# Kernel tuning notes

Measured on AMD Instinct MI355X. Metric: run time of the kernel, lower is better.

## Reference

```python
import jax, jax.numpy as jnp
import numpy as np
from functools import partial

GAMMA = 1.0
LAM = 1.0
N_ITER = 60  # fixed iteration count for the projected-gradient dual fused-lasso solver
GROUP_TOL = 1e-6


def _gfl_solve_row(x, A, lam):
    """Graph fused lasso: argmin_y 0.5||y-x||^2 + lam*sum_ij A_ij |y_i - y_j|.
    Solved by projected gradient ascent on the dual (edge flows z_ij in [-lam*A_ij, lam*A_ij]).
    x: [N], A: [N, N] -> y: [N]
    """
    N = x.shape[0]
    w = lam * A
    step = jnp.asarray(1.0 / (2.0 * N), dtype=x.dtype)

    def body(z, _):
        y = x - jnp.sum(z, axis=1) + jnp.sum(z, axis=0)  # primal from flows
        z = jnp.clip(z + step * (y[:, None] - y[None, :]), -w, w)
        return z, None

    z, _ = jax.lax.scan(body, jnp.zeros_like(A), None, length=N_ITER)
    return x - jnp.sum(z, axis=1) + jnp.sum(z, axis=0)


@partial(jax.custom_vjp, nondiff_argnums=(2,))
def gfusedlasso(x, A, lam):
    # x: [B, N], A: [B, N, N]
    return jax.vmap(_gfl_solve_row, in_axes=(0, 0, None))(x, A, lam)


def _gfl_fwd(x, A, lam):
    out = gfusedlasso(x, A, lam)
    return out, out


def _gfl_bwd(lam, out, g):
    # Faithful to backward_gfusedmax_torch_1D: average grad over groups of equal outputs.
    eq = (jnp.abs(out[:, :, None] - out[:, None, :]) < GROUP_TOL).astype(g.dtype)  # [B,N,N]
    grad_x = jnp.einsum('bij,bj->bi', eq, g) / jnp.sum(eq, axis=2)
    return grad_x, jnp.zeros_like(eq)  # no gradient defined for A (matches torch)


gfusedlasso.defvjp(_gfl_fwd, _gfl_bwd)


def sparsemax(x, axis=-1):
    # torch_sparsemax.forward with gamma=1.0
    N = x.shape[axis]
    x_sorted = jnp.flip(jnp.sort(x, axis=axis), axis=axis)  # descending
    cumsum = jnp.cumsum(x_sorted, axis=axis)
    k = jnp.arange(1, N + 1, dtype=x.dtype)  # broadcast along last axis
    mask = (1.0 + k * x_sorted > cumsum).astype(x.dtype)
    tau = (jnp.sum(x_sorted * mask, axis=axis, keepdims=True) - 1.0) / jnp.sum(mask, axis=axis, keepdims=True)
    return jnp.maximum(x - tau, 0.0)


def setup_inputs() -> dict:
    key = jax.random.key(0)
    kx, ka = jax.random.split(key)
    B, N = 4096, 128
    x = jax.random.normal(kx, (B, N), dtype=jnp.float32)
    A = jax.random.uniform(ka, (B, N, N), dtype=jnp.float32)
    return {"x": x, "A": A}


def reference(x, A):
    # Gfusedmax.forward: x/gamma -> gfusedlasso(lam/gamma) -> sparsemax(gamma=1)
    xg = x / GAMMA
    fused = gfusedlasso(xg, A, LAM / GAMMA)
    return sparsemax(fused, axis=-1)
```

## Files before the change

kernel.cpp:

```cpp
#include <hip/hip_runtime.h>

#define N 128
#define NITER 60
#define PSTR 132

typedef float v2f __attribute__((ext_vector_type(2)));
typedef float v4f __attribute__((ext_vector_type(4)));

__global__ __launch_bounds__(256, 1)
void gfusedmax_kernel(const float* __restrict__ x,
                      const float* __restrict__ A,
                      float* __restrict__ out)
{
    const int b   = blockIdx.x;
    const int tid = threadIdx.x;
    const int tr  = tid >> 4;
    const int tc  = tid & 15;
    const int i0  = tr * 8;
    const int j0  = tc * 8;

    __shared__ float rowpart[16 * PSTR];
    __shared__ float colpart[16 * PSTR];
    __shared__ float yv[N];
    __shared__ float sorted[N];
    __shared__ float red[8];

    const float step = 1.0f / 256.0f;

    v2f w2[8][4];
    v2f z2[8][4];
    const float* Ab = A + (size_t)b * N * N;
    #pragma unroll
    for (int r = 0; r < 8; ++r) {
        const v4f* src = (const v4f*)(Ab + (size_t)(i0 + r) * N + j0);
        v4f p0 = src[0];
        v4f p1 = src[1];
        w2[r][0] = p0.lo; w2[r][1] = p0.hi;
        w2[r][2] = p1.lo; w2[r][3] = p1.hi;
        #pragma unroll
        for (int cp = 0; cp < 4; ++cp) z2[r][cp] = (v2f)0.0f;
    }

    float xi = 0.0f;
    if (tid < N) xi = x[(size_t)b * N + tid];

    v2f pr2[8], pc2[4];
    #pragma unroll
    for (int r = 0; r < 8; ++r) pr2[r] = (v2f)0.0f;
    #pragma unroll
    for (int cp = 0; cp < 4; ++cp) pc2[cp] = (v2f)0.0f;

    float yfin = 0.0f;

    for (int it = 0; it <= NITER; ++it) {
        #pragma unroll
        for (int r = 0; r < 8; ++r)
            rowpart[tc * PSTR + i0 + r] = pr2[r].x + pr2[r].y;
        v2f* cp_dst = (v2f*)&colpart[tr * PSTR + j0];
        #pragma unroll
        for (int cp = 0; cp < 4; ++cp) cp_dst[cp] = pc2[cp];
        __syncthreads();

        if (tid < N) {
            float rs = 0.0f, cs = 0.0f;
            #pragma unroll
            for (int k = 0; k < 16; ++k) rs += rowpart[k * PSTR + tid];
            #pragma unroll
            for (int k = 0; k < 16; ++k) cs += colpart[k * PSTR + tid];
            float y = xi - rs + cs;
            yfin = y;
            yv[tid] = (it == NITER) ? y : step * y;
        }
        __syncthreads();
        if (it == NITER) break;

        v2f drs[8], ec2[4];
        #pragma unroll
        for (int r = 0; r < 8; ++r) drs[r] = (v2f)yv[i0 + r];
        const v2f* yv2 = (const v2f*)yv;
        #pragma unroll
        for (int cp = 0; cp < 4; ++cp) ec2[cp] = yv2[tc * 4 + cp];
        #pragma unroll
        for (int r = 0; r < 8; ++r) pr2[r] = (v2f)0.0f;
        #pragma unroll
        for (int cp = 0; cp < 4; ++cp) pc2[cp] = (v2f)0.0f;
        #pragma unroll
        for (int r = 0; r < 8; ++r) {
            #pragma unroll
            for (int cp = 0; cp < 4; ++cp) {
                v2f t  = (z2[r][cp] + drs[r]) - ec2[cp];
                v2f wv = w2[r][cp];
                v2f zn;
                zn.x = __builtin_amdgcn_fmed3f(t.x, -wv.x, wv.x);
                zn.y = __builtin_amdgcn_fmed3f(t.y, -wv.y, wv.y);
                z2[r][cp] = zn;
                pr2[r]  += zn;
                pc2[cp] += zn;
            }
        }
    }

    float v = yfin;
    if (tid < N) {
        int rk = 0;
        for (int k = 0; k < N; ++k) {
            float u = yv[k];
            rk += (u > v) || (u == v && k < tid);
        }
        sorted[rk] = v;
    }
    __syncthreads();

    float s = 0.0f, csum = 0.0f;
    if (tid < N) {
        s = sorted[tid];
        for (int m = 0; m < N; ++m) {
            float t = sorted[m];
            if (m <= tid) csum += t;
        }
    }
    bool mask = (tid < N) && (1.0f + (float)(tid + 1) * s > csum);
    float aRed = mask ? s : 0.0f;
    float bRed = mask ? 1.0f : 0.0f;
    #pragma unroll
    for (int off = 32; off >= 1; off >>= 1) {
        aRed += __shfl_down(aRed, off, 64);
        bRed += __shfl_down(bRed, off, 64);
    }
    const int wid = tid >> 6;
    if ((tid & 63) == 0) { red[wid * 2] = aRed; red[wid * 2 + 1] = bRed; }
    __syncthreads();
    const float tau = (red[0] + red[2] + red[4] + red[6] - 1.0f)
                    / (red[1] + red[3] + red[5] + red[7]);
    if (tid < N) out[(size_t)b * N + tid] = fmaxf(v - tau, 0.0f);
}

extern "C" void kernel_launch(void* const* d_in, const int* in_sizes, int n_in,
                              void* d_out, int out_size, void* d_ws, size_t ws_size,
                              hipStream_t stream) {
    const float* x = (const float*)d_in[0];
    const float* A = (const float*)d_in[1];
    float* out = (float*)d_out;
    const int B = in_sizes[0] / N;
    gfusedmax_kernel<<<B, 256, 0, stream>>>(x, A, out);
}
```

Before: 877.5 us.

## Interleave two batch rows per block to overlap reductions with clip updates

Each block now handles two batch rows and alternates between them. While one row's z update runs, the same threads gather the other row's row and column partial sums from shared memory, which halves the barriers per row-iteration and hides reduction latency. The sort and sparsemax epilogue uses all 256 threads, one half per row. The cost is doubled register state per thread (z and w for two rows) and half as many blocks, so occupancy and spilling become a risk.

```diff
diff --git a/kernel.cpp b/kernel.cpp
--- a/kernel.cpp
+++ b/kernel.cpp
@@ -2,124 +2,160 @@
 
 #define N 128
 #define NITER 60
-#define PSTR 132
+#define RPS 129
+#define CPS 130
 
 typedef float v2f __attribute__((ext_vector_type(2)));
 typedef float v4f __attribute__((ext_vector_type(4)));
 
-__global__ __launch_bounds__(256, 1)
+template<int Q, int P>
+__device__ __forceinline__ void window_step(
+    v2f (&z2)[2][8][4], const v2f (&w2)[2][8][4],
+    float (&RP)[2][16 * RPS], float (&CP)[2][16 * CPS],
+    float (&YV)[2][N],
+    int tid, int tr, int tc, int i0, int j0,
+    float xiP, bool storeCond, bool rawStore)
+{
+    const float step = 1.0f / 256.0f;
+
+    v2f drs[8], ec2[4], pr2[8], pc2[4];
+    #pragma unroll
+    for (int r = 0; r < 8; ++r) drs[r] = (v2f)YV[Q][i0 + r];
+    const v2f* yv2 = (const v2f*)YV[Q];
+    #pragma unroll
+    for (int cp = 0; cp < 4; ++cp) ec2[cp] = yv2[tc * 4 + cp];
+
+    float rtmp[16], ctmp[16];
+    const int ridx = tid & (N - 1);
+    if (tid < N) {
+        #pragma unroll
+        for (int k = 0; k < 16; ++k) rtmp[k] = RP[P][k * RPS + ridx];
+        #pragma unroll
+        for (int k = 0; k < 16; ++k) ctmp[k] = CP[P][k * CPS + ridx];
+    }
+
+    #pragma unroll
+    for (int r = 0; r < 8; ++r) pr2[r] = (v2f)0.0f;
+    #pragma unroll
+    for (int cp = 0; cp < 4; ++cp) pc2[cp] = (v2f)0.0f;
+
+    #pragma unroll
+    for (int r = 0; r < 8; ++r) {
+        #pragma unroll
+        for (int cp = 0; cp < 4; ++cp) {
+            v2f t  = (z2[Q][r][cp] + drs[r]) - ec2[cp];
+            v2f wv = w2[Q][r][cp];
+            v2f zn;
+            zn.x = __builtin_amdgcn_fmed3f(t.x, -wv.x, wv.x);
+            zn.y = __builtin_amdgcn_fmed3f(t.y, -wv.y, wv.y);
+            z2[Q][r][cp] = zn;
+            pr2[r]  += zn;
+            pc2[cp] += zn;
+        }
+    }
+
+    #pragma unroll
+    for (int r = 0; r < 8; ++r)
+        RP[Q][tc * RPS + i0 + r] = pr2[r].x + pr2[r].y;
+    v2f* cd = (v2f*)&CP[Q][tr * CPS + j0];
+    #pragma unroll
+    for (int cp = 0; cp < 4; ++cp) cd[cp] = pc2[cp];
+
+    if (storeCond) {
+        float rs = 0.0f, cs = 0.0f;
+        #pragma unroll
+        for (int k = 0; k < 16; ++k) rs += rtmp[k];
+        #pragma unroll
+        for (int k = 0; k < 16; ++k) cs += ctmp[k];
+        float y = xiP - rs + cs;
+        YV[P][tid] = rawStore ? y : step * y;
+    }
+}
+
+__global__ __launch_bounds__(256, 2)
 void gfusedmax_kernel(const float* __restrict__ x,
                       const float* __restrict__ A,
                       float* __restrict__ out)
 {
-    const int b   = blockIdx.x;
+    const int b0  = blockIdx.x * 2;
     const int tid = threadIdx.x;
     const int tr  = tid >> 4;
     const int tc  = tid & 15;
     const int i0  = tr * 8;
     const int j0  = tc * 8;
 
-    __shared__ float rowpart[16 * PSTR];
-    __shared__ float colpart[16 * PSTR];
-    __shared__ float yv[N];
-    __shared__ float sorted[N];
-    __shared__ float red[8];
+    __shared__ float RP[2][16 * RPS];
+    __shared__ __align__(16) float CP[2][16 * CPS];
+    __shared__ __align__(16) float YV[2][N];
+    __shared__ float sorted[2][N];
+    __shared__ float red[2][4];
 
     const float step = 1.0f / 256.0f;
 
-    v2f w2[8][4];
-    v2f z2[8][4];
-    const float* Ab = A + (size_t)b * N * N;
+    v2f w2[2][8][4];
+    v2f z2[2][8][4];
     #pragma unroll
-    for (int r = 0; r < 8; ++r) {
-        const v4f* src = (const v4f*)(Ab + (size_t)(i0 + r) * N + j0);
-        v4f p0 = src[0];
-        v4f p1 = src[1];
-        w2[r][0] = p0.lo; w2[r][1] = p0.hi;
-        w2[r][2] = p1.lo; w2[r][3] = p1.hi;
-        #pragma unroll
-        for (int cp = 0; cp < 4; ++cp) z2[r][cp] = (v2f)0.0f;
-    }
-
-    float xi = 0.0f;
-    if (tid < N) xi = x[(size_t)b * N + tid];
-
-    v2f pr2[8], pc2[4];
-    #pragma unroll
-    for (int r = 0; r < 8; ++r) pr2[r] = (v2f)0.0f;
-    #pragma unroll
-    for (int cp = 0; cp < 4; ++cp) pc2[cp] = (v2f)0.0f;
-
-    float yfin = 0.0f;
-
-    for (int it = 0; it <= NITER; ++it) {
-        #pragma unroll
-        for (int r = 0; r < 8; ++r)
-            rowpart[tc * PSTR + i0 + r] = pr2[r].x + pr2[r].y;
-        v2f* cp_dst = (v2f*)&colpart[tr * PSTR + j0];
-        #pragma unroll
-        for (int cp = 0; cp < 4; ++cp) cp_dst[cp] = pc2[cp];
-        __syncthreads();
-
-        if (tid < N) {
-            float rs = 0.0f, cs = 0.0f;
-            #pragma unroll
-            for (int k = 0; k < 16; ++k) rs += rowpart[k * PSTR + tid];
-            #pragma unroll
-            for (int k = 0; k < 16; ++k) cs += colpart[k * PSTR + tid];
-            float y = xi - rs + cs;
-            yfin = y;
-            yv[tid] = (it == NITER) ? y : step * y;
-        }
-        __syncthreads();
-        if (it == NITER) break;
-
-        v2f drs[8], ec2[4];
-        #pragma unroll
-        for (int r = 0; r < 8; ++r) drs[r] = (v2f)yv[i0 + r];
-        const v2f* yv2 = (const v2f*)yv;
-        #pragma unroll
-        for (int cp = 0; cp < 4; ++cp) ec2[cp] = yv2[tc * 4 + cp];
-        #pragma unroll
-        for (int r = 0; r < 8; ++r) pr2[r] = (v2f)0.0f;
-        #pragma unroll
-        for (int cp = 0; cp < 4; ++cp) pc2[cp] = (v2f)0.0f;
+    for (int q = 0; q < 2; ++q) {
+        const float* Ab = A + (size_t)(b0 + q) * N * N;
         #pragma unroll
         for (int r = 0; r < 8; ++r) {
+            const v4f* src = (const v4f*)(Ab + (size_t)(i0 + r) * N + j0);
+            v4f p0 = src[0];
+            v4f p1 = src[1];
+            w2[q][r][0] = p0.lo; w2[q][r][1] = p0.hi;
+            w2[q][r][2] = p1.lo; w2[q][r][3] = p1.hi;
             #pragma unroll
-            for (int cp = 0; cp < 4; ++cp) {
-                v2f t  = (z2[r][cp] + drs[r]) - ec2[cp];
-                v2f wv = w2[r][cp];
-                v2f zn;
-                zn.x = __builtin_amdgcn_fmed3f(t.x, -wv.x, wv.x);
-                zn.y = __builtin_amdgcn_fmed3f(t.y, -wv.y, wv.y);
-                z2[r][cp] = zn;
-                pr2[r]  += zn;
-                pc2[cp] += zn;
-            }
+            for (int cp = 0; cp < 4; ++cp) z2[q][r][cp] = (v2f)0.0f;
         }
     }
 
-    float v = yfin;
+    float xi0 = 0.0f, xi1 = 0.0f;
     if (tid < N) {
-        int rk = 0;
-        for (int k = 0; k < N; ++k) {
-            float u = yv[k];
-            rk += (u > v) || (u == v && k < tid);
-        }
-        sorted[rk] = v;
+        xi0 = x[(size_t)b0 * N + tid];
+        xi1 = x[(size_t)(b0 + 1) * N + tid];
+        YV[0][tid] = step * xi0;
+        YV[1][tid] = step * xi1;
     }
     __syncthreads();
 
-    float s = 0.0f, csum = 0.0f;
+    for (int it = 0; it < NITER; ++it) {
+        window_step<0, 1>(z2, w2, RP, CP, YV, tid, tr, tc, i0, j0,
+                          xi1, (it != 0) && (tid < N), false);
+        __syncthreads();
+        window_step<1, 0>(z2, w2, RP, CP, YV, tid, tr, tc, i0, j0,
+                          xi0, (tid < N), it == NITER - 1);
+        __syncthreads();
+    }
+
     if (tid < N) {
-        s = sorted[tid];
-        for (int m = 0; m < N; ++m) {
-            float t = sorted[m];
-            if (m <= tid) csum += t;
-        }
+        float rs = 0.0f, cs = 0.0f;
+        #pragma unroll
+        for (int k = 0; k < 16; ++k) rs += RP[1][k * RPS + tid];
+        #pragma unroll
+        for (int k = 0; k < 16; ++k) cs += CP[1][k * CPS + tid];
+        YV[1][tid] = xi1 - rs + cs;
     }
-    bool mask = (tid < N) && (1.0f + (float)(tid + 1) * s > csum);
+    __syncthreads();
+
+    const int row = tid >> 7;
+    const int t1  = tid & 127;
+    const float* yrow = YV[row];
+    float v = yrow[t1];
+    int rk = 0;
+    for (int k = 0; k < N; ++k) {
+        float u = yrow[k];
+        rk += (u > v) || (u == v && k < t1);
+    }
+    sorted[row][rk] = v;
+    __syncthreads();
+
+    float s = sorted[row][t1];
+    float csum = 0.0f;
+    for (int m = 0; m < N; ++m) {
+        float t = sorted[row][m];
+        if (m <= t1) csum += t;
+    }
+    bool mask = (1.0f + (float)(t1 + 1) * s > csum);
     float aRed = mask ? s : 0.0f;
     float bRed = mask ? 1.0f : 0.0f;
     #pragma unroll
@@ -127,12 +163,12 @@
         aRed += __shfl_down(aRed, off, 64);
         bRed += __shfl_down(bRed, off, 64);
     }
-    const int wid = tid >> 6;
-    if ((tid & 63) == 0) { red[wid * 2] = aRed; red[wid * 2 + 1] = bRed; }
+    const int wid2 = (tid >> 6) & 1;
+    if ((tid & 63) == 0) { red[row][wid2 * 2] = aRed; red[row][wid2 * 2 + 1] = bRed; }
     __syncthreads();
-    const float tau = (red[0] + red[2] + red[4] + red[6] - 1.0f)
-                    / (red[1] + red[3] + red[5] + red[7]);
-    if (tid < N) out[(size_t)b * N + tid] = fmaxf(v - tau, 0.0f);
+    const float tau = (red[row][0] + red[row][2] - 1.0f)
+                    / (red[row][1] + red[row][3]);
+    out[(size_t)(b0 + row) * N + t1] = fmaxf(v - tau, 0.0f);
 }
 
 extern "C" void kernel_launch(void* const* d_in, const int* in_sizes, int n_in,
@@ -142,5 +178,5 @@
     const float* A = (const float*)d_in[1];
     float* out = (float*)d_out;
     const int B = in_sizes[0] / N;
-    gfusedmax_kernel<<<B, 256, 0, stream>>>(x, A, out);
+    gfusedmax_kernel<<<B / 2, 256, 0, stream>>>(x, A, out);
 }
```

Result: slower. 2.095 ms (+138.8%).
